# Kernel optimization log

Hardware: AMD Instinct MI355X
Metric: run time of the kernel (lower is better)

The kernel has to match this reference:

```python
import jax, jax.numpy as jnp
import numpy as np

N = 50000
E = 640000
F_IN = 96
H1 = 128
H2 = 128
NUM_CLASSES = 256
NGRAM = 3
D1 = 32
L2_EPS = 1e-12


def _prop(xt, src, dst, ew):
    # weighted scatter-add aggregation: out[dst] += ew * xt[src]
    return jax.ops.segment_sum(ew[:, None] * xt[src], dst, num_segments=N)


def _digcn_layer(x, W_mi, W_mo, W_sk, b_mi, b_mo, b_si, b_so, C_in, C_out,
                 ei_in, ew_in, ei_out, ew_out):
    x_sk = x @ W_sk  # skip transform shared by in/out branches
    ic = (_prop(x @ W_mi, ei_in[0], ei_in[1], ew_in) + b_mi
          + _prop(x_sk, ei_in[0], ei_in[1], ew_in) + b_si)
    oc = (_prop(x @ W_mo, ei_out[0], ei_out[1], ew_out) + b_mo
          + _prop(x_sk, ei_out[0], ei_out[1], ew_out) + b_so)
    return C_in * ic + C_out * oc  # C_* are [N,1] vector coefficients


def setup_inputs() -> dict:
    key = jax.random.key(0)
    ks = jax.random.split(key, 32)
    s = 0.05
    d = {
        'x': jax.random.normal(ks[0], (N, F_IN), dtype=jnp.float32),
        'edge_index_in': jax.random.randint(ks[1], (2, E), 0, N, dtype=jnp.int32),
        'edge_weight_in': jax.random.uniform(ks[2], (E,), dtype=jnp.float32),
        'edge_index_out': jax.random.randint(ks[3], (2, E), 0, N, dtype=jnp.int32),
        'edge_weight_out': jax.random.uniform(ks[4], (E,), dtype=jnp.float32),
        'pe_table': jax.random.normal(ks[5], (NGRAM, D1), dtype=jnp.float32) * s,
    }
    dims = [(F_IN, H1), (H1, H1), (H1, H2)]
    ki = 6
    for li, (di, do) in enumerate(dims, start=1):
        d[f'W{li}_main_in'] = jax.random.normal(ks[ki], (di, do), dtype=jnp.float32) * s; ki += 1
        d[f'W{li}_main_out'] = jax.random.normal(ks[ki], (di, do), dtype=jnp.float32) * s; ki += 1
        d[f'W{li}_skip'] = jax.random.normal(ks[ki], (di, do), dtype=jnp.float32) * s; ki += 1
        d[f'b{li}_main_in'] = jax.random.normal(ks[ki], (do,), dtype=jnp.float32) * s; ki += 1
        d[f'b{li}_main_out'] = jax.random.normal(ks[ki], (do,), dtype=jnp.float32) * s; ki += 1
        d[f'b{li}_skip_in'] = jax.random.normal(ks[ki], (do,), dtype=jnp.float32) * s; ki += 1
        d[f'b{li}_skip_out'] = jax.random.normal(ks[ki], (do,), dtype=jnp.float32) * s; ki += 1
        d[f'C{li}_in'] = 1.0 + jax.random.normal(ks[ki], (N, 1), dtype=jnp.float32) * 0.02; ki += 1
        d[f'C{li}_out'] = 1.0 + jax.random.normal(ks[ki], (N, 1), dtype=jnp.float32) * 0.02; ki += 1
    k2 = jax.random.split(ks[ki], 4)
    d['res1_W'] = jax.random.normal(k2[0], (F_IN, H1), dtype=jnp.float32) * s
    d['res1_b'] = jax.random.normal(k2[1], (H1,), dtype=jnp.float32) * s
    d['dec_W'] = jax.random.normal(k2[2], (H2, NUM_CLASSES), dtype=jnp.float32) * s
    d['dec_b'] = jax.random.normal(k2[3], (NUM_CLASSES,), dtype=jnp.float32) * s
    return d


def reference(x, edge_index_in, edge_weight_in, edge_index_out, edge_weight_out, pe_table,
              W1_main_in, W1_main_out, W1_skip, b1_main_in, b1_main_out, b1_skip_in, b1_skip_out, C1_in, C1_out,
              W2_main_in, W2_main_out, W2_skip, b2_main_in, b2_main_out, b2_skip_in, b2_skip_out, C2_in, C2_out,
              W3_main_in, W3_main_out, W3_skip, b3_main_in, b3_main_out, b3_skip_in, b3_skip_out, C3_in, C3_out,
              res1_W, res1_b, dec_W, dec_b):
    # learnable positional encoding: x viewed as [N, ngram, d1] + pe[pos]
    x = (x.reshape(-1, NGRAM, D1) + pe_table[None]).reshape(-1, NGRAM * D1)

    h1 = _digcn_layer(x, W1_main_in, W1_main_out, W1_skip, b1_main_in, b1_main_out,
                      b1_skip_in, b1_skip_out, C1_in, C1_out,
                      edge_index_in, edge_weight_in, edge_index_out, edge_weight_out)
    h1 = jax.nn.relu(h1 + (x @ res1_W + res1_b))  # residual_proj_1 (96 -> 128)

    h2 = _digcn_layer(h1, W2_main_in, W2_main_out, W2_skip, b2_main_in, b2_main_out,
                      b2_skip_in, b2_skip_out, C2_in, C2_out,
                      edge_index_in, edge_weight_in, edge_index_out, edge_weight_out)
    h2 = jax.nn.relu(h2 + h1)  # identity residual (128 == 128)

    h3 = _digcn_layer(h2, W3_main_in, W3_main_out, W3_skip, b3_main_in, b3_main_out,
                      b3_skip_in, b3_skip_out, C3_in, C3_out,
                      edge_index_in, edge_weight_in, edge_index_out, edge_weight_out)
    h3 = h3 + h2  # residual_proj_3 is Identity (hidden1 == hidden2)

    norm = jnp.maximum(jnp.linalg.norm(h3, axis=1, keepdims=True), L2_EPS)
    emb = h3 / norm  # F.normalize, eps=1e-12
    logits = emb @ dec_W + dec_b
    return jax.nn.log_softmax(logits, axis=-1), emb
```

## Files before the change

### kernel.cpp

```cpp
#include <hip/hip_runtime.h>
#include <hip/hip_bf16.h>

typedef unsigned short ushort_t;
typedef __attribute__((ext_vector_type(8))) short bf16x8;
typedef __attribute__((ext_vector_type(4))) float f32x4;

__device__ __forceinline__ float bf2f(ushort_t u) {
    union { unsigned int i; float f; } v; v.i = ((unsigned int)u) << 16; return v.f;
}
__device__ __forceinline__ ushort_t f2bf(float f) {
    unsigned int u = __float_as_uint(f);
    unsigned int r = u + 0x7FFFu + ((u >> 16) & 1u);
    return (ushort_t)(r >> 16);
}
__device__ __forceinline__ float ldf(const void* p, size_t i, int isf) {
    return isf ? ((const float*)p)[i] : bf2f(((const ushort_t*)p)[i]);
}

__global__ void init_k(int* __restrict__ bcntI, int* __restrict__ bcntO,
                       int* __restrict__ bcurI, int* __restrict__ bcurO, int NB,
                       const void* __restrict__ x, int* __restrict__ flag) {
    int i = blockIdx.x * 256 + threadIdx.x;
    if (i < NB) { bcntI[i] = 0; bcntO[i] = 0; bcurI[i] = 0; bcurO[i] = 0; }
    if (blockIdx.x == 0) {
        int t = threadIdx.x;
        const float* xf = (const float*)x;
        int bad = 0;
        for (int k = t; k < 2048; k += 256) {
            unsigned int u = __float_as_uint(xf[k]);
            unsigned int e = (u >> 23) & 0xFFu;
            if (e >= 0xC0u) bad = 1;
        }
        __shared__ int s_bad;
        if (t == 0) s_bad = 0;
        __syncthreads();
        if (bad) atomicOr(&s_bad, 1);
        __syncthreads();
        if (t == 0) flag[0] = s_bad ? 0 : 1;
    }
}


__global__ __launch_bounds__(256) void csr_count_k(
    const int* __restrict__ eiI, const int* __restrict__ eiO,
    int* __restrict__ bcntI, int* __restrict__ bcntO, int E, int nblk) {
    int set = blockIdx.x >= nblk ? 1 : 0;
    int blk = blockIdx.x - set * nblk;
    const int* ei = set ? eiO : eiI;
    int* bcnt = set ? bcntO : bcntI;
    __shared__ unsigned hist[1024];
    int t = threadIdx.x;
    for (int i = t; i < 1024; i += 256) hist[i] = 0;
    __syncthreads();
    int e0 = blk * 8192;
    for (int i = t; i < 8192; i += 256) {
        int e = e0 + i;
        if (e < E) atomicAdd(&hist[((unsigned)ei[E + e]) >> 6], 1u);
    }
    __syncthreads();
    for (int b = t; b < 1024; b += 256) {
        unsigned c = hist[b];
        if (c) atomicAdd(&bcnt[b], (int)c);
    }
}

__global__ __launch_bounds__(256) void csr_scan_k(
    const int* __restrict__ bcntI, const int* __restrict__ bcntO,
    int* __restrict__ bstartI, int* __restrict__ bstartO, int NB, int E) {
    __shared__ int s[256];
    int t = threadIdx.x;
    for (int set = 0; set < 2; ++set) {
        const int* bcnt = set ? bcntO : bcntI;
        int* bstart = set ? bstartO : bstartI;
        int idx = t * 4;
        int v[4];
#pragma unroll
        for (int i = 0; i < 4; ++i) v[i] = (idx + i < NB) ? bcnt[idx + i] : 0;
        int tsum = v[0] + v[1] + v[2] + v[3];
        s[t] = tsum;
        __syncthreads();
        for (int d = 1; d < 256; d <<= 1) {
            int x = (t >= d) ? s[t - d] : 0;
            __syncthreads();
            s[t] += x;
            __syncthreads();
        }
        int run = s[t] - tsum;
#pragma unroll
        for (int i = 0; i < 4; ++i) { if (idx + i < NB) bstart[idx + i] = run; run += v[i]; }
        if (t == 0) bstart[NB] = E;
        __syncthreads();
    }
}

__global__ __launch_bounds__(256) void csr_bin_k(
    const int* __restrict__ eiI, const void* __restrict__ ewI,
    const int* __restrict__ eiO, const void* __restrict__ ewO,
    const int* __restrict__ bstartI, const int* __restrict__ bstartO,
    int* __restrict__ bcurI, int* __restrict__ bcurO,
    uint2* __restrict__ tmpI, uint2* __restrict__ tmpO,
    int E, int nblk, int NB, const int* __restrict__ flagp) {
    int isf = *flagp;
    int set = blockIdx.x >= nblk ? 1 : 0;
    int blk = blockIdx.x - set * nblk;
    const int* ei = set ? eiO : eiI;
    const void* ew = set ? ewO : ewI;
    const int* bstart = set ? bstartO : bstartI;
    int* bcur = set ? bcurO : bcurI;
    uint2* tmp = set ? tmpO : tmpI;
    __shared__ unsigned hist[1024];
    __shared__ unsigned hbase[1024];
    int t = threadIdx.x;
    int e0 = blk * 8192;
    for (int i = t; i < 1024; i += 256) hist[i] = 0;
    __syncthreads();
    for (int i = t; i < 8192; i += 256) {
        int e = e0 + i;
        if (e < E) atomicAdd(&hist[((unsigned)ei[E + e]) >> 6], 1u);
    }
    __syncthreads();
    for (int b = t; b < NB; b += 256) {
        unsigned c = hist[b];
        hbase[b] = c ? (unsigned)atomicAdd(&bcur[b], (int)c) : 0u;
    }
    __syncthreads();
    for (int i = t; i < 1024; i += 256) hist[i] = 0;
    __syncthreads();
    for (int i = t; i < 8192; i += 256) {
        int e = e0 + i;
        if (e < E) {
            unsigned d = (unsigned)ei[E + e];
            unsigned b = d >> 6;
            unsigned r = atomicAdd(&hist[b], 1u);
            unsigned src = (unsigned)ei[e];
            unsigned wb = __float_as_uint(ldf(ew, e, isf));
            tmp[bstart[b] + hbase[b] + r] = make_uint2(src | ((d & 63u) << 26), wb);
        }
    }
}

__global__ __launch_bounds__(256) void csr_final_k(
    const uint2* __restrict__ tmpI, const uint2* __restrict__ tmpO,
    const int* __restrict__ bstartI, const int* __restrict__ bstartO,
    uint2* __restrict__ prI, uint2* __restrict__ prO,
    int* __restrict__ offI, int* __restrict__ offO,
    int N, int E, int NB) {
    int set = blockIdx.x >= NB ? 1 : 0;
    int b = blockIdx.x - set * NB;
    const uint2* tmp = set ? tmpO : tmpI;
    const int* bstart = set ? bstartO : bstartI;
    uint2* pr = set ? prO : prI;
    int* off = set ? offO : offI;
    int s0 = bstart[b], s1 = bstart[b + 1];
    int cnt = s1 - s0;
    __shared__ unsigned ndc[64];
    __shared__ unsigned pref[64];
    __shared__ unsigned ncur[64];
    int t = threadIdx.x;
    if (t < 64) { ndc[t] = 0; ncur[t] = 0; }
    __syncthreads();
    for (int i = t; i < cnt; i += 256)
        atomicAdd(&ndc[tmp[s0 + i].x >> 26], 1u);
    __syncthreads();
    if (t == 0) {
        unsigned run = 0;
        for (int i = 0; i < 64; ++i) { pref[i] = run; run += ndc[i]; }
    }
    __syncthreads();
    if (t < 64) {
        int node = b * 64 + t;
        if (node < N) off[node] = s0 + (int)pref[t];
    }
    if (b == 0 && t == 0) off[N] = E;
    for (int i = t; i < cnt; i += 256) {
        uint2 en = tmp[s0 + i];
        unsigned dl = en.x >> 26;
        unsigned r = atomicAdd(&ncur[dl], 1u);
        pr[s0 + (int)(pref[dl] + r)] = make_uint2(en.x & 0x03FFFFFFu, en.y);
    }
}

struct PrepJob { const void* A; const void* B; ushort_t* dst; int K; int colOff; int cshift; int n; int blkBase; };
struct PrepJobsT { PrepJob j[8]; };
__global__ __launch_bounds__(256) void prep_all_k(PrepJobsT jobs, const int* __restrict__ flagp) {
    int isf = *flagp;
    int b = blockIdx.x;
    int ji = 0;
#pragma unroll
    for (int t = 1; t < 8; ++t) if (b >= jobs.j[t].blkBase) ji = t;
    PrepJob jb = jobs.j[ji];
    int i = (b - jb.blkBase) * 256 + threadIdx.x;
    if (i >= jb.n) return;
    int cmask = (1 << jb.cshift) - 1;
    int k = i >> jb.cshift, c = i & cmask;
    int Cw = cmask + 1;
    float v = ldf(jb.A, (size_t)k * Cw + c, isf);
    if (jb.B) v += ldf(jb.B, (size_t)k * Cw + c, isf);
    jb.dst[(size_t)(jb.colOff + c) * jb.K + k] = f2bf(v);
}

struct BiasJob { const void* a; const void* b; float* dst; int n; };
struct BiasJobs { BiasJob j[8]; };
__global__ void prep_bias_k(BiasJobs jobs, const int* __restrict__ flagp) {
    int isf = *flagp;
    BiasJob jb = jobs.j[blockIdx.x];
    int t = threadIdx.x;
    if (t < jb.n) {
        float v = ldf(jb.a, t, isf);
        if (jb.b) v += ldf(jb.b, t, isf);
        jb.dst[t] = v;
    }
}

template<int K, int DOUT>
__global__ __launch_bounds__(256) void gemm_mfma_k(
    const ushort_t* __restrict__ A, const ushort_t* __restrict__ Wt,
    ushort_t* __restrict__ Y, int M) {
    constexpr int NT = DOUT / 16;
    int tid = threadIdx.x;
    int wave = tid >> 6, lane = tid & 63;
    int q = lane >> 4, l15 = lane & 15;
    int arow = blockIdx.x * 64 + wave * 16 + l15;
    int rowc = arow < M ? arow : M - 1;
    f32x4 acc[NT];
#pragma unroll
    for (int t = 0; t < NT; ++t) acc[t] = (f32x4){0.f, 0.f, 0.f, 0.f};
#pragma unroll
    for (int kc = 0; kc < K; kc += 32) {
        bf16x8 a = *(const bf16x8*)(A + (size_t)rowc * K + kc + q * 8);
#pragma unroll
        for (int t = 0; t < NT; ++t) {
            bf16x8 b = *(const bf16x8*)(Wt + (size_t)(t * 16 + l15) * K + kc + q * 8);
            acc[t] = __builtin_amdgcn_mfma_f32_16x16x32_bf16(a, b, acc[t], 0, 0, 0);
        }
    }
    int outRowBase = blockIdx.x * 64 + wave * 16 + q * 4;
#pragma unroll
    for (int t = 0; t < NT; ++t) {
        int col = t * 16 + l15;
#pragma unroll
        for (int i = 0; i < 4; ++i) {
            int r = outRowBase + i;
            if (r < M) Y[(size_t)r * DOUT + col] = f2bf(acc[t][i]);
        }
    }
}

__global__ __launch_bounds__(256) void gemm_mfma_x_k(
    const void* __restrict__ X, const ushort_t* __restrict__ Wt,
    ushort_t* __restrict__ Y, int M, const void* __restrict__ pe,
    const int* __restrict__ flagp) {
    constexpr int K = 96, DOUT = 384, NT = DOUT / 16;
    __shared__ float pes[96];
    int isf = *flagp;
    int tid = threadIdx.x;
    if (tid < 96) pes[tid] = ldf(pe, tid, isf);
    __syncthreads();
    int wave = tid >> 6, lane = tid & 63;
    int q = lane >> 4, l15 = lane & 15;
    int arow = blockIdx.x * 64 + wave * 16 + l15;
    int rowc = arow < M ? arow : M - 1;
    f32x4 acc[NT];
#pragma unroll
    for (int t = 0; t < NT; ++t) acc[t] = (f32x4){0.f, 0.f, 0.f, 0.f};
#pragma unroll
    for (int kc = 0; kc < K; kc += 32) {
        float va[8];
        size_t base = (size_t)rowc * K + kc + q * 8;
        if (isf) {
            float4 u0 = *(const float4*)((const float*)X + base);
            float4 u1 = *(const float4*)((const float*)X + base + 4);
            va[0] = u0.x; va[1] = u0.y; va[2] = u0.z; va[3] = u0.w;
            va[4] = u1.x; va[5] = u1.y; va[6] = u1.z; va[7] = u1.w;
        } else {
            const ushort_t* xp = (const ushort_t*)X + base;
#pragma unroll
            for (int i = 0; i < 8; ++i) va[i] = bf2f(xp[i]);
        }
        bf16x8 a;
        short* ap = (short*)&a;
#pragma unroll
        for (int i = 0; i < 8; ++i) ap[i] = (short)f2bf(va[i] + pes[kc + q * 8 + i]);
#pragma unroll
        for (int t = 0; t < NT; ++t) {
            bf16x8 b = *(const bf16x8*)(Wt + (size_t)(t * 16 + l15) * K + kc + q * 8);
            acc[t] = __builtin_amdgcn_mfma_f32_16x16x32_bf16(a, b, acc[t], 0, 0, 0);
        }
    }
    int outRowBase = blockIdx.x * 64 + wave * 16 + q * 4;
#pragma unroll
    for (int t = 0; t < NT; ++t) {
        int col = t * 16 + l15;
#pragma unroll
        for (int i = 0; i < 4; ++i) {
            int r = outRowBase + i;
            if (r < M) Y[(size_t)r * DOUT + col] = f2bf(acc[t][i]);
        }
    }
}

__device__ __forceinline__ void accum8(float* acc, uint4 v, float w) {
    unsigned u[4] = {v.x, v.y, v.z, v.w};
#pragma unroll
    for (int i = 0; i < 4; ++i) {
        acc[2 * i]     = fmaf(w, __uint_as_float(u[i] << 16), acc[2 * i]);
        acc[2 * i + 1] = fmaf(w, __uint_as_float(u[i] & 0xFFFF0000u), acc[2 * i + 1]);
    }
}

__global__ __launch_bounds__(256) void prop_combine_k(
    const ushort_t* __restrict__ Y, int ldY,
    const int* __restrict__ offI, const uint2* __restrict__ prI,
    const int* __restrict__ offO, const uint2* __restrict__ prO,
    const void* __restrict__ Cin, const void* __restrict__ Cout,
    const float* __restrict__ bin, const float* __restrict__ bout,
    const ushort_t* __restrict__ res, int ldR, int colR, const float* __restrict__ res_b,
    ushort_t* __restrict__ H, int M, int relu, const int* __restrict__ flagp) {
    int isf = *flagp;
    int node = blockIdx.x * 4 + (threadIdx.x >> 6);
    int lane = threadIdx.x & 63;
    if (node >= M) return;
    int half = lane >> 5;
    int subq = (lane >> 4) & 1;
    int li   = lane & 15;
    int eI0 = offI[node], eI1 = offI[node + 1];
    int eO0 = offO[node], eO1 = offO[node + 1];
    int e0 = half ? eO0 : eI0;
    int e1 = half ? eO1 : eI1;
    const uint2* pairs = half ? prO : prI;
    const ushort_t* rowbase = Y + half * 128 + li * 8;
    int lenMax = max(eI1 - eI0, eO1 - eO0);
    float acc[8];
#pragma unroll
    for (int k = 0; k < 8; ++k) acc[k] = 0.f;
    for (int it = 0; it < lenMax; it += 4) {
        int eeA = e0 + it + subq;
        int eeB = eeA + 2;
        bool mA = eeA < e1, mB = eeB < e1;
        uint2 pa, pb;
        uint4 va, vb;
        if (mA) { pa = pairs[eeA]; va = *(const uint4*)(rowbase + (size_t)pa.x * ldY); }
        if (mB) { pb = pairs[eeB]; vb = *(const uint4*)(rowbase + (size_t)pb.x * ldY); }
        if (mA) accum8(acc, va, __uint_as_float(pa.y));
        if (mB) accum8(acc, vb, __uint_as_float(pb.y));
    }
    float other[8];
#pragma unroll
    for (int k = 0; k < 8; ++k) {
        acc[k] += __shfl_xor(acc[k], 16, 64);
        other[k] = __shfl_xor(acc[k], 32, 64);
    }
    int j = li * 8;
    float ci = ldf(Cin, node, isf), co = ldf(Cout, node, isf);
    uint4 rv = *(const uint4*)(res + (size_t)node * ldR + colR + j);
    float4 b0 = *(const float4*)(bin + j);
    float4 b1 = *(const float4*)(bin + j + 4);
    float4 c0 = *(const float4*)(bout + j);
    float4 c1 = *(const float4*)(bout + j + 4);
    float binv[8]  = {b0.x, b0.y, b0.z, b0.w, b1.x, b1.y, b1.z, b1.w};
    float boutv[8] = {c0.x, c0.y, c0.z, c0.w, c1.x, c1.y, c1.z, c1.w};
    float rbv[8] = {0.f, 0.f, 0.f, 0.f, 0.f, 0.f, 0.f, 0.f};
    if (res_b) {
        float4 r0 = *(const float4*)(res_b + j);
        float4 r1 = *(const float4*)(res_b + j + 4);
        rbv[0] = r0.x; rbv[1] = r0.y; rbv[2] = r0.z; rbv[3] = r0.w;
        rbv[4] = r1.x; rbv[5] = r1.y; rbv[6] = r1.z; rbv[7] = r1.w;
    }
    unsigned rw[4] = {rv.x, rv.y, rv.z, rv.w};
    float vo[8];
#pragma unroll
    for (int k = 0; k < 8; ++k) {
        float aiv = half ? other[k] : acc[k];
        float aov = half ? acc[k] : other[k];
        float r = (k & 1) ? __uint_as_float(rw[k >> 1] & 0xFFFF0000u)
                          : __uint_as_float(rw[k >> 1] << 16);
        float v = ci * (aiv + binv[k]) + co * (aov + boutv[k]) + r + rbv[k];
        if (relu) v = fmaxf(v, 0.f);
        vo[k] = v;
    }
    if ((lane >> 4) == 0) {
        uint4 outv;
        unsigned* op = (unsigned*)&outv;
#pragma unroll
        for (int k = 0; k < 4; ++k)
            op[k] = ((unsigned)f2bf(vo[2 * k + 1]) << 16) | (unsigned)f2bf(vo[2 * k]);
        *(uint4*)(H + (size_t)node * 128 + j) = outv;
    }
}

__global__ __launch_bounds__(256) void decoder_mfma_k(
    const ushort_t* __restrict__ h3, const ushort_t* __restrict__ Wdt,
    const float* __restrict__ biasDec, void* __restrict__ d_out, int M,
    const int* __restrict__ flagp) {
    __shared__ ushort_t embLds[64 * 136];
    __shared__ float sb[256];
    int isf = *flagp;
    int tid = threadIdx.x;
    sb[tid] = biasDec[tid];
    int rowBase = blockIdx.x * 64;
    {
        int r = tid >> 2;
        int c0 = (tid & 3) * 32;
        int grow = rowBase + r;
        uint4 u[4] = {};
        if (grow < M) {
            const uint4* p = (const uint4*)(h3 + (size_t)grow * 128 + c0);
            u[0] = p[0]; u[1] = p[1]; u[2] = p[2]; u[3] = p[3];
        }
        float v[32];
#pragma unroll
        for (int b = 0; b < 4; ++b) {
            unsigned w[4] = {u[b].x, u[b].y, u[b].z, u[b].w};
#pragma unroll
            for (int i = 0; i < 4; ++i) {
                v[b * 8 + 2 * i]     = bf2f((ushort_t)(w[i] & 0xffffu));
                v[b * 8 + 2 * i + 1] = bf2f((ushort_t)(w[i] >> 16));
            }
        }
        float ss = 0.f;
#pragma unroll
        for (int i = 0; i < 32; ++i) ss += v[i] * v[i];
        ss += __shfl_xor(ss, 1, 64);
        ss += __shfl_xor(ss, 2, 64);
        float inv = 1.0f / fmaxf(sqrtf(ss), 1e-12f);
#pragma unroll
        for (int i = 0; i < 32; ++i) v[i] *= inv;
        unsigned* lp = (unsigned*)&embLds[r * 136 + c0];
#pragma unroll
        for (int i = 0; i < 16; ++i)
            lp[i] = ((unsigned)f2bf(v[2 * i + 1]) << 16) | (unsigned)f2bf(v[2 * i]);
        if (grow < M) {
            if (isf) {
                float* op = (float*)d_out + (size_t)M * 256 + (size_t)grow * 128 + c0;
#pragma unroll
                for (int i = 0; i < 32; ++i) op[i] = v[i];
            } else {
                unsigned* op = (unsigned*)((ushort_t*)d_out + (size_t)M * 256 + (size_t)grow * 128 + c0);
#pragma unroll
                for (int i = 0; i < 16; ++i)
                    op[i] = ((unsigned)f2bf(v[2 * i + 1]) << 16) | (unsigned)f2bf(v[2 * i]);
            }
        }
    }
    __syncthreads();
    int wave = tid >> 6, lane = tid & 63, q = lane >> 4, l15 = lane & 15;
    f32x4 acc[16];
#pragma unroll
    for (int t = 0; t < 16; ++t) acc[t] = (f32x4){0.f, 0.f, 0.f, 0.f};
    int ldsRow = wave * 16 + l15;
#pragma unroll
    for (int kc = 0; kc < 128; kc += 32) {
        bf16x8 a = *(const bf16x8*)(&embLds[ldsRow * 136 + kc + q * 8]);
#pragma unroll
        for (int t = 0; t < 16; ++t) {
            bf16x8 b = *(const bf16x8*)(Wdt + (size_t)(t * 16 + l15) * 128 + kc + q * 8);
            acc[t] = __builtin_amdgcn_mfma_f32_16x16x32_bf16(a, b, acc[t], 0, 0, 0);
        }
    }
#pragma unroll
    for (int t = 0; t < 16; ++t) {
        float b = sb[t * 16 + l15];
        acc[t][0] += b; acc[t][1] += b; acc[t][2] += b; acc[t][3] += b;
    }
#pragma unroll
    for (int i = 0; i < 4; ++i) {
        int grow = rowBase + wave * 16 + q * 4 + i;
        float mx = acc[0][i];
#pragma unroll
        for (int t = 1; t < 16; ++t) mx = fmaxf(mx, acc[t][i]);
        mx = fmaxf(mx, __shfl_xor(mx, 1, 64));
        mx = fmaxf(mx, __shfl_xor(mx, 2, 64));
        mx = fmaxf(mx, __shfl_xor(mx, 4, 64));
        mx = fmaxf(mx, __shfl_xor(mx, 8, 64));
        float sm = 0.f;
#pragma unroll
        for (int t = 0; t < 16; ++t) sm += __expf(acc[t][i] - mx);
        sm += __shfl_xor(sm, 1, 64);
        sm += __shfl_xor(sm, 2, 64);
        sm += __shfl_xor(sm, 4, 64);
        sm += __shfl_xor(sm, 8, 64);
        float offv = mx + __logf(sm);
        if (grow < M) {
            if (isf) {
                float* op = (float*)d_out + (size_t)grow * 256 + l15;
#pragma unroll
                for (int t = 0; t < 16; ++t) op[t * 16] = acc[t][i] - offv;
            } else {
                ushort_t* op = (ushort_t*)d_out + (size_t)grow * 256 + l15;
#pragma unroll
                for (int t = 0; t < 16; ++t) op[t * 16] = f2bf(acc[t][i] - offv);
            }
        }
    }
}

extern "C" void kernel_launch(void* const* d_in, const int* in_sizes, int n_in,
                              void* d_out, int out_size, void* d_ws, size_t ws_size,
                              hipStream_t stream) {
    const int N = in_sizes[0] / 96;
    const int E = in_sizes[2];

    const void* x      = d_in[0];
    const int*  ei_in  = (const int*)d_in[1];
    const void* ew_in  = d_in[2];
    const int*  ei_out = (const int*)d_in[3];
    const void* ew_out = d_in[4];
    const void* pe     = d_in[5];

    const void *W_mi[3], *W_mo[3], *W_sk[3], *b_mi[3], *b_mo[3], *b_si[3], *b_so[3], *C_i[3], *C_o[3];
    for (int l = 0; l < 3; ++l) {
        int base = 6 + l * 9;
        W_mi[l] = d_in[base + 0];
        W_mo[l] = d_in[base + 1];
        W_sk[l] = d_in[base + 2];
        b_mi[l] = d_in[base + 3];
        b_mo[l] = d_in[base + 4];
        b_si[l] = d_in[base + 5];
        b_so[l] = d_in[base + 6];
        C_i[l]  = d_in[base + 7];
        C_o[l]  = d_in[base + 8];
    }
    const void* res1_W = d_in[33];
    const void* res1_b = d_in[34];
    const void* dec_W  = d_in[35];
    const void* dec_b  = d_in[36];

    char* ws = (char*)d_ws;
    size_t off = 0;
    auto alloc = [&](size_t bytes) -> void* {
        void* p = ws + off;
        off = (off + bytes + 255) & ~(size_t)255;
        return p;
    };
    const int NB = (N + 63) / 64;
    int*   flag    = (int*)alloc(4);
    int*   off_in  = (int*)alloc((size_t)(N + 1) * 4);
    int*   off_out = (int*)alloc((size_t)(N + 1) * 4);
    uint2* pr_in   = (uint2*)alloc((size_t)E * 8);
    uint2* pr_out  = (uint2*)alloc((size_t)E * 8);
    int*   bcntI   = (int*)alloc((size_t)NB * 4);
    int*   bcntO   = (int*)alloc((size_t)NB * 4);
    int*   bcurI   = (int*)alloc((size_t)NB * 4);
    int*   bcurO   = (int*)alloc((size_t)NB * 4);
    int*   bstartI = (int*)alloc((size_t)(NB + 1) * 4);
    int*   bstartO = (int*)alloc((size_t)(NB + 1) * 4);
    ushort_t* Wt1  = (ushort_t*)alloc((size_t)384 * 96 * 2);
    ushort_t* Wt2  = (ushort_t*)alloc((size_t)256 * 128 * 2);
    ushort_t* Wt3  = (ushort_t*)alloc((size_t)256 * 128 * 2);
    ushort_t* Wdt  = (ushort_t*)alloc((size_t)256 * 128 * 2);
    float* biasBlk = (float*)alloc((size_t)1152 * 4);
    float* bin1 = biasBlk, *bout1 = biasBlk + 128, *bin2 = biasBlk + 256, *bout2 = biasBlk + 384;
    float* bin3 = biasBlk + 512, *bout3 = biasBlk + 640, *res1b = biasBlk + 768, *decb = biasBlk + 896;
    ushort_t* Yb  = (ushort_t*)alloc((size_t)N * 384 * 2);
    ushort_t* H1  = (ushort_t*)alloc((size_t)N * 128 * 2);
    ushort_t* H2  = (ushort_t*)alloc((size_t)N * 128 * 2);
    ushort_t* H3  = H1;
    uint2* tmpI = (uint2*)Yb;
    uint2* tmpO = tmpI + E;

    {
        int g = (NB + 255) / 256;
        init_k<<<g, 256, 0, stream>>>(bcntI, bcntO, bcurI, bcurO, NB, x, flag);
    }

    const int EB = 8192;
    int nblk = (E + EB - 1) / EB;
    csr_count_k<<<2 * nblk, 256, 0, stream>>>(ei_in, ei_out, bcntI, bcntO, E, nblk);
    csr_scan_k<<<1, 256, 0, stream>>>(bcntI, bcntO, bstartI, bstartO, NB, E);
    csr_bin_k<<<2 * nblk, 256, 0, stream>>>(ei_in, ew_in, ei_out, ew_out,
        bstartI, bstartO, bcurI, bcurO, tmpI, tmpO, E, nblk, NB, flag);
    csr_final_k<<<2 * NB, 256, 0, stream>>>(tmpI, tmpO, bstartI, bstartO,
        pr_in, pr_out, off_in, off_out, N, E, NB);

    {
        PrepJobsT pj;
        pj.j[0] = {W_mi[0], W_sk[0], Wt1, 96, 0,   7, 128 * 96, 0};
        pj.j[1] = {W_mo[0], W_sk[0], Wt1, 96, 128, 7, 128 * 96, 48};
        pj.j[2] = {res1_W, nullptr,  Wt1, 96, 256, 7, 128 * 96, 96};
        pj.j[3] = {W_mi[1], W_sk[1], Wt2, 128, 0,   7, 128 * 128, 144};
        pj.j[4] = {W_mo[1], W_sk[1], Wt2, 128, 128, 7, 128 * 128, 208};
        pj.j[5] = {W_mi[2], W_sk[2], Wt3, 128, 0,   7, 128 * 128, 272};
        pj.j[6] = {W_mo[2], W_sk[2], Wt3, 128, 128, 7, 128 * 128, 336};
        pj.j[7] = {dec_W, nullptr, Wdt, 128, 0, 8, 32768, 400};
        prep_all_k<<<528, 256, 0, stream>>>(pj, flag);
    }
    {
        BiasJobs jb;
        jb.j[0] = {b_mi[0], b_si[0], bin1, 128};
        jb.j[1] = {b_mo[0], b_so[0], bout1, 128};
        jb.j[2] = {b_mi[1], b_si[1], bin2, 128};
        jb.j[3] = {b_mo[1], b_so[1], bout2, 128};
        jb.j[4] = {b_mi[2], b_si[2], bin3, 128};
        jb.j[5] = {b_mo[2], b_so[2], bout3, 128};
        jb.j[6] = {res1_b, nullptr, res1b, 128};
        jb.j[7] = {dec_b, nullptr, decb, 256};
        prep_bias_k<<<8, 256, 0, stream>>>(jb, flag);
    }

    int gBlocks = (N + 63) / 64;
    int pgrid = (N + 3) / 4;

    gemm_mfma_x_k<<<gBlocks, 256, 0, stream>>>(x, Wt1, Yb, N, pe, flag);
    prop_combine_k<<<pgrid, 256, 0, stream>>>(Yb, 384,
        off_in, pr_in, off_out, pr_out,
        C_i[0], C_o[0], bin1, bout1, Yb, 384, 256, res1b, H1, N, 1, flag);
    gemm_mfma_k<128, 256><<<gBlocks, 256, 0, stream>>>(H1, Wt2, Yb, N);
    prop_combine_k<<<pgrid, 256, 0, stream>>>(Yb, 256,
        off_in, pr_in, off_out, pr_out,
        C_i[1], C_o[1], bin2, bout2, H1, 128, 0, (const float*)nullptr, H2, N, 1, flag);
    gemm_mfma_k<128, 256><<<gBlocks, 256, 0, stream>>>(H2, Wt3, Yb, N);
    prop_combine_k<<<pgrid, 256, 0, stream>>>(Yb, 256,
        off_in, pr_in, off_out, pr_out,
        C_i[2], C_o[2], bin3, bout3, H2, 128, 0, (const float*)nullptr, H3, N, 0, flag);
    decoder_mfma_k<<<gBlocks, 256, 0, stream>>>(H3, Wdt, decb, d_out, N, flag);
}
```

Before: 559.2 us.

## Aggregate before transform: sparse-propagate inputs, then GEMM with stacked weights and fused epilogue

Reorders each layer so the sparse in/out aggregation runs on the narrow input features (96 or 128 wide) first, scaled by the C coefficients. A GEMM over the concatenated [agg_in, agg_out, (x)] operand with vertically stacked weights then produces the layer output, with bias, residual and ReLU fused into its epilogue. This halves the width of the gathered rows per edge in layer 1 (96 vs 384 cols) and layers 2-3 (128 vs 256), cutting the gather traffic. The cost is a doubled GEMM K dimension, an extra pass that materializes x+pe, and a different rounding order, since the C coefficients are applied before the bf16 matmul.

Result: no change. 555.3 us (-0.7%).

```diff
diff --git a/kernel.cpp b/kernel.cpp
--- a/kernel.cpp
+++ b/kernel.cpp
@@ -180,7 +180,7 @@
     }
 }
 
-struct PrepJob { const void* A; const void* B; ushort_t* dst; int K; int colOff; int cshift; int n; int blkBase; };
+struct PrepJob { const void* A; const void* B; ushort_t* dst; int K; int colOff; int kOff; int cshift; int n; int blkBase; };
 struct PrepJobsT { PrepJob j[8]; };
 __global__ __launch_bounds__(256) void prep_all_k(PrepJobsT jobs, const int* __restrict__ flagp) {
     int isf = *flagp;
@@ -196,7 +196,7 @@
     int Cw = cmask + 1;
     float v = ldf(jb.A, (size_t)k * Cw + c, isf);
     if (jb.B) v += ldf(jb.B, (size_t)k * Cw + c, isf);
-    jb.dst[(size_t)(jb.colOff + c) * jb.K + k] = f2bf(v);
+    jb.dst[(size_t)(jb.colOff + c) * jb.K + jb.kOff + k] = f2bf(v);
 }
 
 struct BiasJob { const void* a; const void* b; float* dst; int n; };
@@ -212,11 +212,108 @@
     }
 }
 
-template<int K, int DOUT>
-__global__ __launch_bounds__(256) void gemm_mfma_k(
+__global__ __launch_bounds__(256) void xpe_k(const void* __restrict__ X, const void* __restrict__ pe,
+                                             ushort_t* __restrict__ Xpe, int total4,
+                                             const int* __restrict__ flagp) {
+    __shared__ float pes[96];
+    int isf = *flagp;
+    if (threadIdx.x < 96) pes[threadIdx.x] = ldf(pe, threadIdx.x, isf);
+    __syncthreads();
+    int i = blockIdx.x * 256 + threadIdx.x;
+    if (i >= total4) return;
+    int n = i / 24, c4 = (i % 24) * 4;
+    size_t base = (size_t)n * 96 + c4;
+    float v[4];
+    if (isf) {
+        float4 u = *(const float4*)((const float*)X + base);
+        v[0] = u.x; v[1] = u.y; v[2] = u.z; v[3] = u.w;
+    } else {
+        const ushort_t* xp = (const ushort_t*)X + base;
+#pragma unroll
+        for (int j = 0; j < 4; ++j) v[j] = bf2f(xp[j]);
+    }
+#pragma unroll
+    for (int j = 0; j < 4; ++j) v[j] += pes[c4 + j];
+    uint2 o;
+    o.x = ((unsigned)f2bf(v[1]) << 16) | (unsigned)f2bf(v[0]);
+    o.y = ((unsigned)f2bf(v[3]) << 16) | (unsigned)f2bf(v[2]);
+    *(uint2*)(Xpe + base) = o;
+}
+
+__device__ __forceinline__ void accum8(float* acc, uint4 v, float w) {
+    unsigned u[4] = {v.x, v.y, v.z, v.w};
+#pragma unroll
+    for (int i = 0; i < 4; ++i) {
+        acc[2 * i]     = fmaf(w, __uint_as_float(u[i] << 16), acc[2 * i]);
+        acc[2 * i + 1] = fmaf(w, __uint_as_float(u[i] & 0xFFFF0000u), acc[2 * i + 1]);
+    }
+}
+
+__global__ __launch_bounds__(256) void agg_k(
+    const ushort_t* __restrict__ X, int NC, int NLI,
+    const int* __restrict__ offI, const uint2* __restrict__ prI,
+    const int* __restrict__ offO, const uint2* __restrict__ prO,
+    const void* __restrict__ Cin, const void* __restrict__ Cout,
+    int copyX, ushort_t* __restrict__ A, int ldA,
+    int M, const int* __restrict__ flagp) {
+    int isf = *flagp;
+    int node = blockIdx.x * 4 + (threadIdx.x >> 6);
+    int lane = threadIdx.x & 63;
+    if (node >= M) return;
+    int half = lane >> 5;
+    int subq = (lane >> 4) & 1;
+    int li = lane & 15;
+    bool act = li < NLI;
+    int eI0 = offI[node], eI1 = offI[node + 1];
+    int eO0 = offO[node], eO1 = offO[node + 1];
+    int e0 = half ? eO0 : eI0;
+    int e1 = half ? eO1 : eI1;
+    const uint2* pairs = half ? prO : prI;
+    const ushort_t* rowbase = X + li * 8;
+    int lenMax = max(eI1 - eI0, eO1 - eO0);
+    float acc[8];
+#pragma unroll
+    for (int k = 0; k < 8; ++k) acc[k] = 0.f;
+    for (int it = 0; it < lenMax; it += 4) {
+        int eeA = e0 + it + subq;
+        int eeB = eeA + 2;
+        bool mA = act && (eeA < e1), mB = act && (eeB < e1);
+        uint2 pa, pb;
+        uint4 va, vb;
+        if (mA) { pa = pairs[eeA]; va = *(const uint4*)(rowbase + (size_t)pa.x * NC); }
+        if (mB) { pb = pairs[eeB]; vb = *(const uint4*)(rowbase + (size_t)pb.x * NC); }
+        if (mA) accum8(acc, va, __uint_as_float(pa.y));
+        if (mB) accum8(acc, vb, __uint_as_float(pb.y));
+    }
+#pragma unroll
+    for (int k = 0; k < 8; ++k) acc[k] += __shfl_xor(acc[k], 16, 64);
+    float c = ldf(half ? Cout : Cin, node, isf);
+    int qtr = lane >> 4;
+    if (act && (qtr == 0 || qtr == 2)) {
+        int band = (qtr == 2) ? NC : 0;
+        uint4 o;
+        unsigned* op = (unsigned*)&o;
+#pragma unroll
+        for (int k2 = 0; k2 < 4; ++k2)
+            op[k2] = ((unsigned)f2bf(c * acc[2 * k2 + 1]) << 16) | (unsigned)f2bf(c * acc[2 * k2]);
+        *(uint4*)(A + (size_t)node * ldA + band + li * 8) = o;
+    }
+    if (copyX && act && qtr == 1) {
+        uint4 v = *(const uint4*)(X + (size_t)node * NC + li * 8);
+        *(uint4*)(A + (size_t)node * ldA + 2 * NC + li * 8) = v;
+    }
+}
+
+template<int K, int RELU, int HASRES>
+__global__ __launch_bounds__(256) void gemm_combine_k(
     const ushort_t* __restrict__ A, const ushort_t* __restrict__ Wt,
-    ushort_t* __restrict__ Y, int M) {
-    constexpr int NT = DOUT / 16;
+    const void* __restrict__ Cin, const void* __restrict__ Cout,
+    const float* __restrict__ bin, const float* __restrict__ bout,
+    const float* __restrict__ badd,
+    const ushort_t* __restrict__ Hres,
+    ushort_t* __restrict__ Hout, int M, const int* __restrict__ flagp) {
+    constexpr int NT = 8;
+    int isf = *flagp;
     int tid = threadIdx.x;
     int wave = tid >> 6, lane = tid & 63;
     int q = lane >> 4, l15 = lane & 15;
@@ -236,155 +333,19 @@
     }
     int outRowBase = blockIdx.x * 64 + wave * 16 + q * 4;
 #pragma unroll
-    for (int t = 0; t < NT; ++t) {
-        int col = t * 16 + l15;
-#pragma unroll
-        for (int i = 0; i < 4; ++i) {
-            int r = outRowBase + i;
-            if (r < M) Y[(size_t)r * DOUT + col] = f2bf(acc[t][i]);
-        }
-    }
-}
-
-__global__ __launch_bounds__(256) void gemm_mfma_x_k(
-    const void* __restrict__ X, const ushort_t* __restrict__ Wt,
-    ushort_t* __restrict__ Y, int M, const void* __restrict__ pe,
-    const int* __restrict__ flagp) {
-    constexpr int K = 96, DOUT = 384, NT = DOUT / 16;
-    __shared__ float pes[96];
-    int isf = *flagp;
-    int tid = threadIdx.x;
-    if (tid < 96) pes[tid] = ldf(pe, tid, isf);
-    __syncthreads();
-    int wave = tid >> 6, lane = tid & 63;
-    int q = lane >> 4, l15 = lane & 15;
-    int arow = blockIdx.x * 64 + wave * 16 + l15;
-    int rowc = arow < M ? arow : M - 1;
-    f32x4 acc[NT];
-#pragma unroll
-    for (int t = 0; t < NT; ++t) acc[t] = (f32x4){0.f, 0.f, 0.f, 0.f};
-#pragma unroll
-    for (int kc = 0; kc < K; kc += 32) {
-        float va[8];
-        size_t base = (size_t)rowc * K + kc + q * 8;
-        if (isf) {
-            float4 u0 = *(const float4*)((const float*)X + base);
-            float4 u1 = *(const float4*)((const float*)X + base + 4);
-            va[0] = u0.x; va[1] = u0.y; va[2] = u0.z; va[3] = u0.w;
-            va[4] = u1.x; va[5] = u1.y; va[6] = u1.z; va[7] = u1.w;
-        } else {
-            const ushort_t* xp = (const ushort_t*)X + base;
-#pragma unroll
-            for (int i = 0; i < 8; ++i) va[i] = bf2f(xp[i]);
-        }
-        bf16x8 a;
-        short* ap = (short*)&a;
-#pragma unroll
-        for (int i = 0; i < 8; ++i) ap[i] = (short)f2bf(va[i] + pes[kc + q * 8 + i]);
+    for (int i = 0; i < 4; ++i) {
+        int r = outRowBase + i;
+        if (r >= M) continue;
+        float ci = ldf(Cin, r, isf), co = ldf(Cout, r, isf);
 #pragma unroll
         for (int t = 0; t < NT; ++t) {
-            bf16x8 b = *(const bf16x8*)(Wt + (size_t)(t * 16 + l15) * K + kc + q * 8);
-            acc[t] = __builtin_amdgcn_mfma_f32_16x16x32_bf16(a, b, acc[t], 0, 0, 0);
-        }
-    }
-    int outRowBase = blockIdx.x * 64 + wave * 16 + q * 4;
-#pragma unroll
-    for (int t = 0; t < NT; ++t) {
-        int col = t * 16 + l15;
-#pragma unroll
-        for (int i = 0; i < 4; ++i) {
-            int r = outRowBase + i;
-            if (r < M) Y[(size_t)r * DOUT + col] = f2bf(acc[t][i]);
-        }
-    }
-}
-
-__device__ __forceinline__ void accum8(float* acc, uint4 v, float w) {
-    unsigned u[4] = {v.x, v.y, v.z, v.w};
-#pragma unroll
-    for (int i = 0; i < 4; ++i) {
-        acc[2 * i]     = fmaf(w, __uint_as_float(u[i] << 16), acc[2 * i]);
-        acc[2 * i + 1] = fmaf(w, __uint_as_float(u[i] & 0xFFFF0000u), acc[2 * i + 1]);
-    }
-}
-
-__global__ __launch_bounds__(256) void prop_combine_k(
-    const ushort_t* __restrict__ Y, int ldY,
-    const int* __restrict__ offI, const uint2* __restrict__ prI,
-    const int* __restrict__ offO, const uint2* __restrict__ prO,
-    const void* __restrict__ Cin, const void* __restrict__ Cout,
-    const float* __restrict__ bin, const float* __restrict__ bout,
-    const ushort_t* __restrict__ res, int ldR, int colR, const float* __restrict__ res_b,
-    ushort_t* __restrict__ H, int M, int relu, const int* __restrict__ flagp) {
-    int isf = *flagp;
-    int node = blockIdx.x * 4 + (threadIdx.x >> 6);
-    int lane = threadIdx.x & 63;
-    if (node >= M) return;
-    int half = lane >> 5;
-    int subq = (lane >> 4) & 1;
-    int li   = lane & 15;
-    int eI0 = offI[node], eI1 = offI[node + 1];
-    int eO0 = offO[node], eO1 = offO[node + 1];
-    int e0 = half ? eO0 : eI0;
-    int e1 = half ? eO1 : eI1;
-    const uint2* pairs = half ? prO : prI;
-    const ushort_t* rowbase = Y + half * 128 + li * 8;
-    int lenMax = max(eI1 - eI0, eO1 - eO0);
-    float acc[8];
-#pragma unroll
-    for (int k = 0; k < 8; ++k) acc[k] = 0.f;
-    for (int it = 0; it < lenMax; it += 4) {
-        int eeA = e0 + it + subq;
-        int eeB = eeA + 2;
-        bool mA = eeA < e1, mB = eeB < e1;
-        uint2 pa, pb;
-        uint4 va, vb;
-        if (mA) { pa = pairs[eeA]; va = *(const uint4*)(rowbase + (size_t)pa.x * ldY); }
-        if (mB) { pb = pairs[eeB]; vb = *(const uint4*)(rowbase + (size_t)pb.x * ldY); }
-        if (mA) accum8(acc, va, __uint_as_float(pa.y));
-        if (mB) accum8(acc, vb, __uint_as_float(pb.y));
-    }
-    float other[8];
-#pragma unroll
-    for (int k = 0; k < 8; ++k) {
-        acc[k] += __shfl_xor(acc[k], 16, 64);
-        other[k] = __shfl_xor(acc[k], 32, 64);
-    }
-    int j = li * 8;
-    float ci = ldf(Cin, node, isf), co = ldf(Cout, node, isf);
-    uint4 rv = *(const uint4*)(res + (size_t)node * ldR + colR + j);
-    float4 b0 = *(const float4*)(bin + j);
-    float4 b1 = *(const float4*)(bin + j + 4);
-    float4 c0 = *(const float4*)(bout + j);
-    float4 c1 = *(const float4*)(bout + j + 4);
-    float binv[8]  = {b0.x, b0.y, b0.z, b0.w, b1.x, b1.y, b1.z, b1.w};
-    float boutv[8] = {c0.x, c0.y, c0.z, c0.w, c1.x, c1.y, c1.z, c1.w};
-    float rbv[8] = {0.f, 0.f, 0.f, 0.f, 0.f, 0.f, 0.f, 0.f};
-    if (res_b) {
-        float4 r0 = *(const float4*)(res_b + j);
-        float4 r1 = *(const float4*)(res_b + j + 4);
-        rbv[0] = r0.x; rbv[1] = r0.y; rbv[2] = r0.z; rbv[3] = r0.w;
-        rbv[4] = r1.x; rbv[5] = r1.y; rbv[6] = r1.z; rbv[7] = r1.w;
-    }
-    unsigned rw[4] = {rv.x, rv.y, rv.z, rv.w};
-    float vo[8];
-#pragma unroll
-    for (int k = 0; k < 8; ++k) {
-        float aiv = half ? other[k] : acc[k];
-        float aov = half ? acc[k] : other[k];
-        float r = (k & 1) ? __uint_as_float(rw[k >> 1] & 0xFFFF0000u)
-                          : __uint_as_float(rw[k >> 1] << 16);
-        float v = ci * (aiv + binv[k]) + co * (aov + boutv[k]) + r + rbv[k];
-        if (relu) v = fmaxf(v, 0.f);
-        vo[k] = v;
-    }
-    if ((lane >> 4) == 0) {
-        uint4 outv;
-        unsigned* op = (unsigned*)&outv;
-#pragma unroll
-        for (int k = 0; k < 4; ++k)
-            op[k] = ((unsigned)f2bf(vo[2 * k + 1]) << 16) | (unsigned)f2bf(vo[2 * k]);
-        *(uint4*)(H + (size_t)node * 128 + j) = outv;
+            int col = t * 16 + l15;
+            float v = acc[t][i] + ci * bin[col] + co * bout[col];
+            if (badd) v += badd[col];
+            if (HASRES) v += bf2f(Hres[(size_t)r * 128 + col]);
+            if (RELU) v = fmaxf(v, 0.f);
+            Hout[(size_t)r * 128 + col] = f2bf(v);
+        }
     }
 }
 
@@ -544,18 +505,21 @@
     int*   bcurO   = (int*)alloc((size_t)NB * 4);
     int*   bstartI = (int*)alloc((size_t)(NB + 1) * 4);
     int*   bstartO = (int*)alloc((size_t)(NB + 1) * 4);
-    ushort_t* Wt1  = (ushort_t*)alloc((size_t)384 * 96 * 2);
-    ushort_t* Wt2  = (ushort_t*)alloc((size_t)256 * 128 * 2);
-    ushort_t* Wt3  = (ushort_t*)alloc((size_t)256 * 128 * 2);
+    ushort_t* Wt1  = (ushort_t*)alloc((size_t)128 * 288 * 2);
+    ushort_t* Wt2  = (ushort_t*)alloc((size_t)128 * 256 * 2);
+    ushort_t* Wt3  = (ushort_t*)alloc((size_t)128 * 256 * 2);
     ushort_t* Wdt  = (ushort_t*)alloc((size_t)256 * 128 * 2);
     float* biasBlk = (float*)alloc((size_t)1152 * 4);
     float* bin1 = biasBlk, *bout1 = biasBlk + 128, *bin2 = biasBlk + 256, *bout2 = biasBlk + 384;
     float* bin3 = biasBlk + 512, *bout3 = biasBlk + 640, *res1b = biasBlk + 768, *decb = biasBlk + 896;
-    ushort_t* Yb  = (ushort_t*)alloc((size_t)N * 384 * 2);
+    ushort_t* Xpe = (ushort_t*)alloc((size_t)N * 96 * 2);
+    size_t abytes = (size_t)N * 288 * 2;
+    size_t tbytes = (size_t)E * 16;
+    ushort_t* A   = (ushort_t*)alloc(abytes > tbytes ? abytes : tbytes);
     ushort_t* H1  = (ushort_t*)alloc((size_t)N * 128 * 2);
     ushort_t* H2  = (ushort_t*)alloc((size_t)N * 128 * 2);
     ushort_t* H3  = H1;
-    uint2* tmpI = (uint2*)Yb;
+    uint2* tmpI = (uint2*)A;
     uint2* tmpO = tmpI + E;
 
     {
@@ -574,14 +538,14 @@
 
     {
         PrepJobsT pj;
-        pj.j[0] = {W_mi[0], W_sk[0], Wt1, 96, 0,   7, 128 * 96, 0};
-        pj.j[1] = {W_mo[0], W_sk[0], Wt1, 96, 128, 7, 128 * 96, 48};
-        pj.j[2] = {res1_W, nullptr,  Wt1, 96, 256, 7, 128 * 96, 96};
-        pj.j[3] = {W_mi[1], W_sk[1], Wt2, 128, 0,   7, 128 * 128, 144};
-        pj.j[4] = {W_mo[1], W_sk[1], Wt2, 128, 128, 7, 128 * 128, 208};
-        pj.j[5] = {W_mi[2], W_sk[2], Wt3, 128, 0,   7, 128 * 128, 272};
-        pj.j[6] = {W_mo[2], W_sk[2], Wt3, 128, 128, 7, 128 * 128, 336};
-        pj.j[7] = {dec_W, nullptr, Wdt, 128, 0, 8, 32768, 400};
+        pj.j[0] = {W_mi[0], W_sk[0], Wt1, 288, 0, 0,   7, 128 * 96, 0};
+        pj.j[1] = {W_mo[0], W_sk[0], Wt1, 288, 0, 96,  7, 128 * 96, 48};
+        pj.j[2] = {res1_W, nullptr,  Wt1, 288, 0, 192, 7, 128 * 96, 96};
+        pj.j[3] = {W_mi[1], W_sk[1], Wt2, 256, 0, 0,   7, 128 * 128, 144};
+        pj.j[4] = {W_mo[1], W_sk[1], Wt2, 256, 0, 128, 7, 128 * 128, 208};
+        pj.j[5] = {W_mi[2], W_sk[2], Wt3, 256, 0, 0,   7, 128 * 128, 272};
+        pj.j[6] = {W_mo[2], W_sk[2], Wt3, 256, 0, 128, 7, 128 * 128, 336};
+        pj.j[7] = {dec_W, nullptr, Wdt, 128, 0, 0, 8, 32768, 400};
         prep_all_k<<<528, 256, 0, stream>>>(pj, flag);
     }
     {
@@ -597,20 +561,25 @@
         prep_bias_k<<<8, 256, 0, stream>>>(jb, flag);
     }
 
+    {
+        int total4 = N * 24;
+        xpe_k<<<(total4 + 255) / 256, 256, 0, stream>>>(x, pe, Xpe, total4, flag);
+    }
+
     int gBlocks = (N + 63) / 64;
     int pgrid = (N + 3) / 4;
 
-    gemm_mfma_x_k<<<gBlocks, 256, 0, stream>>>(x, Wt1, Yb, N, pe, flag);
-    prop_combine_k<<<pgrid, 256, 0, stream>>>(Yb, 384,
-        off_in, pr_in, off_out, pr_out,
-        C_i[0], C_o[0], bin1, bout1, Yb, 384, 256, res1b, H1, N, 1, flag);
-    gemm_mfma_k<128, 256><<<gBlocks, 256, 0, stream>>>(H1, Wt2, Yb, N);
-    prop_combine_k<<<pgrid, 256, 0, stream>>>(Yb, 256,
-        off_in, pr_in, off_out, pr_out,
-        C_i[1], C_o[1], bin2, bout2, H1, 128, 0, (const float*)nullptr, H2, N, 1, flag);
-    gemm_mfma_k<128, 256><<<gBlocks, 256, 0, stream>>>(H2, Wt3, Yb, N);
-    prop_combine_k<<<pgrid, 256, 0, stream>>>(Yb, 256,
-        off_in, pr_in, off_out, pr_out,
-        C_i[2], C_o[2], bin3, bout3, H2, 128, 0, (const float*)nullptr, H3, N, 0, flag);
+    agg_k<<<pgrid, 256, 0, stream>>>(Xpe, 96, 12, off_in, pr_in, off_out, pr_out,
+        C_i[0], C_o[0], 1, A, 288, N, flag);
+    gemm_combine_k<288, 1, 0><<<gBlocks, 256, 0, stream>>>(A, Wt1,
+        C_i[0], C_o[0], bin1, bout1, res1b, (const ushort_t*)nullptr, H1, N, flag);
+    agg_k<<<pgrid, 256, 0, stream>>>(H1, 128, 16, off_in, pr_in, off_out, pr_out,
+        C_i[1], C_o[1], 0, A, 256, N, flag);
+    gemm_combine_k<256, 1, 1><<<gBlocks, 256, 0, stream>>>(A, Wt2,
+        C_i[1], C_o[1], bin2, bout2, (const float*)nullptr, H1, H2, N, flag);
+    agg_k<<<pgrid, 256, 0, stream>>>(H2, 128, 16, off_in, pr_in, off_out, pr_out,
+        C_i[2], C_o[2], 0, A, 256, N, flag);
+    gemm_combine_k<256, 0, 1><<<gBlocks, 256, 0, stream>>>(A, Wt3,
+        C_i[2], C_o[2], bin3, bout3, (const float*)nullptr, H2, H3, N, flag);
     decoder_mfma_k<<<gBlocks, 256, 0, stream>>>(H3, Wdt, decb, d_out, N, flag);
 }
```
